# Kernel optimization log

Hardware: AMD Instinct MI355X
Metric: run time of the kernel (lower is better)

## Reference

```python
import jax, jax.numpy as jnp
import numpy as np

B, S, H, D = 8, 4096, 1024, 256  # batch, seq, hidden_size, state_size


def setup_inputs() -> dict:
    key = jax.random.key(0)
    ks = jax.random.split(key, 4)
    scale_in = 1.0 / np.sqrt(H)
    scale_st = 1.0 / np.sqrt(D)
    return {
        "x": jax.random.normal(ks[0], (B, S, H), dtype=jnp.float32),
        "W_in": jax.random.normal(ks[1], (H, D), dtype=jnp.float32) * scale_in,
        "b_in": jnp.zeros((D,), dtype=jnp.float32),
        "W_state": jax.random.normal(ks[2], (D, D), dtype=jnp.float32) * scale_st,
        "b_state": jnp.zeros((D,), dtype=jnp.float32),
        "W_out": jax.random.normal(ks[3], (D, H), dtype=jnp.float32) * scale_st,
        "b_out": jnp.zeros((H,), dtype=jnp.float32),
    }


def reference(x, W_in, b_in, W_state, b_state, W_out, b_out):
    # Precompute input projection for all timesteps in one big GEMM: [B,S,D]
    inp = jnp.einsum("bsh,hd->bsd", x, W_in) + b_in

    def step(state, inp_t):
        # state: [B,D], inp_t: [B,D]
        state = jnp.tanh(inp_t + state @ W_state + b_state)
        return state, state

    state0 = jnp.zeros((x.shape[0], W_state.shape[0]), dtype=x.dtype)
    # scan over time axis -> states: [S,B,D]
    _, states = jax.lax.scan(step, state0, jnp.swapaxes(inp, 0, 1))
    # output projection: [S,B,H] -> [B,S,H]
    out = jnp.einsum("sbd,dh->sbh", states, W_out) + b_out
    return jnp.swapaxes(out, 0, 1)
```

## Files before the change

kernel.cpp:

```cpp
#include <hip/hip_runtime.h>
#include <stdint.h>


typedef float v4f __attribute__((ext_vector_type(4)));
typedef __bf16 bf16x4 __attribute__((ext_vector_type(4)));
typedef __bf16 bf16x8 __attribute__((ext_vector_type(8)));
typedef _Float16 h8 __attribute__((ext_vector_type(8)));

#define BARRIER_LGKM() asm volatile("s_waitcnt lgkmcnt(0)\n\ts_barrier" ::: "memory")

#define GLOAD_LDS16(g, l)                                                    \
  __builtin_amdgcn_global_load_lds(                                          \
      (const __attribute__((address_space(1))) void*)(g),                    \
      (__attribute__((address_space(3))) void*)(l), 16, 0, 0)

__global__ void cvt_f32_bf16_x4(const float* __restrict__ in,
                                __bf16* __restrict__ out, int n4) {
  int i = blockIdx.x * blockDim.x + threadIdx.x;
  if (i >= n4) return;
  v4f v = ((const v4f*)in)[i];
  bf16x4 o;
  o.x = (__bf16)v.x; o.y = (__bf16)v.y; o.z = (__bf16)v.z; o.w = (__bf16)v.w;
  ((bf16x4*)out)[i] = o;
}

__global__ void transpose_cvt(const float* __restrict__ in,
                              __bf16* __restrict__ out, int K, int N) {
  int i = blockIdx.x * blockDim.x + threadIdx.x;
  if (i >= K * N) return;
  int k = i / N;
  int n = i - k * N;
  out[(size_t)n * K + k] = (__bf16)in[i];
}

__global__ __launch_bounds__(256) void gemm_tile(
    const __bf16* __restrict__ A,
    const __bf16* __restrict__ Bt,
    const float* __restrict__ bias,
    float* __restrict__ C,
    int M, int N, int K) {
  const int tid = threadIdx.x;
  const int lane = tid & 63;
  const int w = tid >> 6;
  const int wr = w >> 1, wc = w & 1;
  const int r = lane & 15, q = lane >> 4;

  const int nbn = N >> 7;
  const int mb = blockIdx.x / nbn;
  const int nb = blockIdx.x - mb * nbn;
  const int m0 = mb << 7, n0 = nb << 7;

  __shared__ __align__(16) char lds[2][16384];

  const __bf16* gA[2];
  const __bf16* gB[2];
  int loff[2];
#pragma unroll
  for (int j = 0; j < 2; ++j) {
    int o = (w * 2 + j) * 1024 + lane * 16;
    int row = o >> 6;
    int s = (o >> 4) & 3;
    int ss = s ^ ((row >> 1) & 3);
    gA[j] = A + (size_t)(m0 + row) * K + ss * 8;
    gB[j] = Bt + (size_t)(n0 + row) * K + ss * 8;
    loff[j] = (w * 2 + j) * 1024;
  }

  const int slot = (q ^ ((r >> 1) & 3)) * 16;
  int aoff[4], boff[4];
#pragma unroll
  for (int i = 0; i < 4; ++i) {
    aoff[i] = (wr * 64 + i * 16 + r) * 64 + slot;
    boff[i] = 8192 + (wc * 64 + i * 16 + r) * 64 + slot;
  }

  v4f acc[4][4];
#pragma unroll
  for (int mi = 0; mi < 4; ++mi)
#pragma unroll
    for (int ni = 0; ni < 4; ++ni) acc[mi][ni] = (v4f){0.f, 0.f, 0.f, 0.f};

  const int NK = K >> 5;
#pragma unroll
  for (int j = 0; j < 2; ++j) {
    GLOAD_LDS16(gA[j], lds[0] + loff[j]);
    GLOAD_LDS16(gB[j], lds[0] + 8192 + loff[j]);
  }

  for (int kt = 0; kt < NK; ++kt) {
    __syncthreads();
    if (kt + 1 < NK) {
      const int b = (kt + 1) & 1;
      const int ke = (kt + 1) * 32;
#pragma unroll
      for (int j = 0; j < 2; ++j) {
        GLOAD_LDS16(gA[j] + ke, lds[b] + loff[j]);
        GLOAD_LDS16(gB[j] + ke, lds[b] + 8192 + loff[j]);
      }
    }
    const char* Lb = lds[kt & 1];
    bf16x8 af[4], bf[4];
#pragma unroll
    for (int i = 0; i < 4; ++i) af[i] = *(const bf16x8*)(Lb + aoff[i]);
#pragma unroll
    for (int i = 0; i < 4; ++i) bf[i] = *(const bf16x8*)(Lb + boff[i]);
#pragma unroll
    for (int mi = 0; mi < 4; ++mi)
#pragma unroll
      for (int ni = 0; ni < 4; ++ni)
        acc[mi][ni] = __builtin_amdgcn_mfma_f32_16x16x32_bf16(
            af[mi], bf[ni], acc[mi][ni], 0, 0, 0);
  }

  float bv[4];
#pragma unroll
  for (int ni = 0; ni < 4; ++ni) bv[ni] = bias[n0 + wc * 64 + ni * 16 + r];
#pragma unroll
  for (int mi = 0; mi < 4; ++mi) {
    int rowb = m0 + wr * 64 + mi * 16 + q * 4;
#pragma unroll
    for (int ni = 0; ni < 4; ++ni) {
      int col = n0 + wc * 64 + ni * 16 + r;
      float* cp = C + (size_t)rowb * N + col;
#pragma unroll
      for (int i = 0; i < 4; ++i) cp[(size_t)i * N] = acc[mi][ni][i] + bv[ni];
    }
  }
}

__global__ __launch_bounds__(512, 2) void scan_mfma(
    const float* __restrict__ inp,
    const float* __restrict__ Wst,
    const float* __restrict__ b_state,
    __bf16* __restrict__ states,
    int S) {
  const int tid = threadIdx.x;
  const int l = tid & 63;
  const int q = l >> 4;
  const int r = l & 15;
  const int w = tid >> 6;
  const int b = blockIdx.x;

  __shared__ __align__(16) _Float16 sbuf[2][256];

  h8 bwA[8], bwB[8];
#pragma unroll
  for (int c = 0; c < 8; ++c) {
#pragma unroll
    for (int i = 0; i < 8; ++i) {
      const float* wp = Wst + (size_t)(32 * c + 8 * q + i) * 256 + 32 * w + r;
      bwA[c][i] = (_Float16)wp[0];
      bwB[c][i] = (_Float16)wp[16];
    }
  }

  const int col = 32 * w + 16 * (q & 1) + r;
  const float bst = b_state[col];
  const float* inpb = inp + (size_t)b * S * 256;
  __bf16* stb = states + (size_t)b * S * 256;

  if (tid < 256) sbuf[0][tid] = (_Float16)0.f;
  float u_cur = inpb[col];
  float u_nxt = inpb[256 + col];
  __syncthreads();

  int cur = 0;
  for (int t = 0; t < S; ++t) {
    float u_n2 = 0.f;
    if (t + 2 < S) u_n2 = inpb[(size_t)(t + 2) * 256 + col];

    const h8* sp = (const h8*)sbuf[cur];
    h8 af[8];
#pragma unroll
    for (int c = 0; c < 8; ++c) af[c] = sp[4 * c + q];

    v4f a0 = {0.f, 0.f, 0.f, 0.f};
    v4f a1 = a0;
#pragma unroll
    for (int c = 0; c < 8; ++c) {
      a0 = __builtin_amdgcn_mfma_f32_16x16x32_f16(af[c], bwA[c], a0, 0, 0, 0);
      a1 = __builtin_amdgcn_mfma_f32_16x16x32_f16(af[c], bwB[c], a1, 0, 0, 0);
    }
    float x = ((q & 1) ? a1[0] : a0[0]) + u_cur + bst;

    float e = exp2f(2.885390082f * x);
    float sn = 1.f - 2.f * __builtin_amdgcn_rcpf(e + 1.f);

    cur ^= 1;
    if (q < 2) {
      sbuf[cur][col] = (_Float16)sn;
      stb[(size_t)t * 256 + col] = (__bf16)sn;
    }
    u_cur = u_nxt;
    u_nxt = u_n2;
    BARRIER_LGKM();
  }
}

extern "C" void kernel_launch(void* const* d_in, const int* in_sizes, int n_in,
                              void* d_out, int out_size, void* d_ws,
                              size_t ws_size, hipStream_t stream) {
  const float* x       = (const float*)d_in[0];
  const float* W_in    = (const float*)d_in[1];
  const float* b_in    = (const float*)d_in[2];
  const float* W_state = (const float*)d_in[3];
  const float* b_state = (const float*)d_in[4];
  const float* W_out   = (const float*)d_in[5];
  const float* b_out   = (const float*)d_in[6];
  float* out = (float*)d_out;

  const int B = 8, S = 4096, H = 1024, D = 256;
  const int M = B * S;

  char* ws = (char*)d_ws;
  float*  inp    = (float*)(ws + 0);
  __bf16* states = (__bf16*)(ws + 33554432);
  __bf16* xb     = (__bf16*)(ws + 50331648);
  __bf16* WinT   = (__bf16*)(ws + 117440512);
  __bf16* WoutT  = (__bf16*)(ws + 117964800);

  cvt_f32_bf16_x4<<<(M * H / 4 + 255) / 256, 256, 0, stream>>>(x, xb, M * H / 4);
  transpose_cvt<<<(H * D + 255) / 256, 256, 0, stream>>>(W_in, WinT, H, D);
  transpose_cvt<<<(D * H + 255) / 256, 256, 0, stream>>>(W_out, WoutT, D, H);

  gemm_tile<<<(M / 128) * (D / 128), 256, 0, stream>>>(xb, WinT, b_in, inp, M, D, H);

  scan_mfma<<<B, 512, 0, stream>>>(inp, W_state, b_state, states, S);

  gemm_tile<<<(M / 128) * (H / 128), 256, 0, stream>>>(states, WoutT, b_out, out, M, H, D);
}
```

Baseline: 2.113 ms.

## Split scan recurrence across 16 waves with one 16-column tile each

The sequential scan kernel now runs 1024 threads (16 waves) per batch element instead of 8. Each wave owns a single 16-column output tile, and the eight MFMAs are split across two independent accumulators, shortening the dependent MFMA chain per timestep. The intent is to cut per-step latency on the serial recurrence. The cost is a barrier across more waves every step and fewer lanes doing writes. The GEMM variable rename is cosmetic.

After: 2.106 ms. Within noise of the previous version (-0.3%).

```diff
diff --git a/kernel.cpp b/kernel.cpp
--- a/kernel.cpp
+++ b/kernel.cpp
@@ -90,12 +90,12 @@
   for (int kt = 0; kt < NK; ++kt) {
     __syncthreads();
     if (kt + 1 < NK) {
-      const int b = (kt + 1) & 1;
+      const int bb = (kt + 1) & 1;
       const int ke = (kt + 1) * 32;
 #pragma unroll
       for (int j = 0; j < 2; ++j) {
-        GLOAD_LDS16(gA[j] + ke, lds[b] + loff[j]);
-        GLOAD_LDS16(gB[j] + ke, lds[b] + 8192 + loff[j]);
+        GLOAD_LDS16(gA[j] + ke, lds[bb] + loff[j]);
+        GLOAD_LDS16(gB[j] + ke, lds[bb] + 8192 + loff[j]);
       }
     }
     const char* Lb = lds[kt & 1];
@@ -128,7 +128,7 @@
   }
 }
 
-__global__ __launch_bounds__(512, 2) void scan_mfma(
+__global__ __launch_bounds__(1024) void scan_mfma(
     const float* __restrict__ inp,
     const float* __restrict__ Wst,
     const float* __restrict__ b_state,
@@ -143,18 +143,15 @@
 
   __shared__ __align__(16) _Float16 sbuf[2][256];
 
-  h8 bwA[8], bwB[8];
+  h8 bw[8];
 #pragma unroll
   for (int c = 0; c < 8; ++c) {
 #pragma unroll
-    for (int i = 0; i < 8; ++i) {
-      const float* wp = Wst + (size_t)(32 * c + 8 * q + i) * 256 + 32 * w + r;
-      bwA[c][i] = (_Float16)wp[0];
-      bwB[c][i] = (_Float16)wp[16];
-    }
-  }
-
-  const int col = 32 * w + 16 * (q & 1) + r;
+    for (int i = 0; i < 8; ++i)
+      bw[c][i] = (_Float16)Wst[(size_t)(32 * c + 8 * q + i) * 256 + 16 * w + r];
+  }
+
+  const int col = 16 * w + r;
   const float bst = b_state[col];
   const float* inpb = inp + (size_t)b * S * 256;
   __bf16* stb = states + (size_t)b * S * 256;
@@ -174,20 +171,20 @@
 #pragma unroll
     for (int c = 0; c < 8; ++c) af[c] = sp[4 * c + q];
 
-    v4f a0 = {0.f, 0.f, 0.f, 0.f};
-    v4f a1 = a0;
-#pragma unroll
-    for (int c = 0; c < 8; ++c) {
-      a0 = __builtin_amdgcn_mfma_f32_16x16x32_f16(af[c], bwA[c], a0, 0, 0, 0);
-      a1 = __builtin_amdgcn_mfma_f32_16x16x32_f16(af[c], bwB[c], a1, 0, 0, 0);
-    }
-    float x = ((q & 1) ? a1[0] : a0[0]) + u_cur + bst;
+    v4f accE = {0.f, 0.f, 0.f, 0.f};
+    v4f accO = accE;
+#pragma unroll
+    for (int c = 0; c < 4; ++c) {
+      accE = __builtin_amdgcn_mfma_f32_16x16x32_f16(af[2 * c],     bw[2 * c],     accE, 0, 0, 0);
+      accO = __builtin_amdgcn_mfma_f32_16x16x32_f16(af[2 * c + 1], bw[2 * c + 1], accO, 0, 0, 0);
+    }
+    float x = accE[0] + accO[0] + u_cur + bst;
 
     float e = exp2f(2.885390082f * x);
     float sn = 1.f - 2.f * __builtin_amdgcn_rcpf(e + 1.f);
 
     cur ^= 1;
-    if (q < 2) {
+    if (q == 0) {
       sbuf[cur][col] = (_Float16)sn;
       stb[(size_t)t * 256 + col] = (__bf16)sn;
     }
@@ -225,7 +222,7 @@
 
   gemm_tile<<<(M / 128) * (D / 128), 256, 0, stream>>>(xb, WinT, b_in, inp, M, D, H);
 
-  scan_mfma<<<B, 512, 0, stream>>>(inp, W_state, b_state, states, S);
+  scan_mfma<<<B, 1024, 0, stream>>>(inp, W_state, b_state, states, S);
 
   gemm_tile<<<(M / 128) * (H / 128), 256, 0, stream>>>(states, WoutT, b_out, out, M, H, D);
 }
```

## Fuse input GEMM, scan and output GEMM into one persistent kernel with flags

Applied to the files above, without the earlier changes.

Replaces the three separate launches (input-projection GEMM, sequential scan, output-projection GEMM) with one persistent kernel. Eight blocks run the scan while the other blocks pull work items from an atomic counter, producing input-projection chunks ahead of the scan and consuming finished state chunks for the output GEMM. Progress and readiness are passed through global flags with acquire/release fences. This hides the two GEMMs behind the latency-bound scan. Worker blocks sharing a CU with a scan block are told to exit so they do not slow it, at the cost of spin-wait and fence overhead in the scan loop every 128 steps.

Measured after the change: 2.293 ms. 1.09x slower.

```diff
diff --git a/kernel.cpp b/kernel.cpp
--- a/kernel.cpp
+++ b/kernel.cpp
@@ -13,6 +13,22 @@
   __builtin_amdgcn_global_load_lds(                                          \
       (const __attribute__((address_space(1))) void*)(g),                    \
       (__attribute__((address_space(3))) void*)(l), 16, 0, 0)
+
+#define GETREG_HWID  __builtin_amdgcn_s_getreg(0xF804)
+#define GETREG_XCCID __builtin_amdgcn_s_getreg(0xF814)
+
+#define AT_LOAD(p)     __hip_atomic_load((p), __ATOMIC_RELAXED, __HIP_MEMORY_SCOPE_AGENT)
+#define AT_STORE(p, v) __hip_atomic_store((p), (v), __ATOMIC_RELAXED, __HIP_MEMORY_SCOPE_AGENT)
+#define AT_ADD(p, v)   __hip_atomic_fetch_add((p), (v), __ATOMIC_RELAXED, __HIP_MEMORY_SCOPE_AGENT)
+#define FENCE_ACQ() __builtin_amdgcn_fence(__ATOMIC_ACQUIRE, "agent")
+#define FENCE_REL() __builtin_amdgcn_fence(__ATOMIC_RELEASE, "agent")
+
+#define CTL_NEXT 0
+#define CTL_REG  1
+#define CTL_PROG 2
+#define CTL_SCU  10
+#define CTL_EXIT 18
+#define CTL_G1   32
 
 __global__ void cvt_f32_bf16_x4(const float* __restrict__ in,
                                 __bf16* __restrict__ out, int n4) {
@@ -33,24 +49,16 @@
   out[(size_t)n * K + k] = (__bf16)in[i];
 }
 
-__global__ __launch_bounds__(256) void gemm_tile(
-    const __bf16* __restrict__ A,
-    const __bf16* __restrict__ Bt,
-    const float* __restrict__ bias,
-    float* __restrict__ C,
-    int M, int N, int K) {
-  const int tid = threadIdx.x;
+__global__ void zero_ctl(uint32_t* p) { p[threadIdx.x] = 0; }
+
+__device__ __forceinline__ void gemm128(
+    const __bf16* __restrict__ A, const __bf16* __restrict__ Bt,
+    const float* __restrict__ bias, float* __restrict__ C,
+    int N, int K, int m0, int n0, char* lds, int tid) {
   const int lane = tid & 63;
   const int w = tid >> 6;
   const int wr = w >> 1, wc = w & 1;
   const int r = lane & 15, q = lane >> 4;
-
-  const int nbn = N >> 7;
-  const int mb = blockIdx.x / nbn;
-  const int nb = blockIdx.x - mb * nbn;
-  const int m0 = mb << 7, n0 = nb << 7;
-
-  __shared__ __align__(16) char lds[2][16384];
 
   const __bf16* gA[2];
   const __bf16* gB[2];
@@ -83,22 +91,22 @@
   const int NK = K >> 5;
 #pragma unroll
   for (int j = 0; j < 2; ++j) {
-    GLOAD_LDS16(gA[j], lds[0] + loff[j]);
-    GLOAD_LDS16(gB[j], lds[0] + 8192 + loff[j]);
+    GLOAD_LDS16(gA[j], lds + loff[j]);
+    GLOAD_LDS16(gB[j], lds + 8192 + loff[j]);
   }
 
   for (int kt = 0; kt < NK; ++kt) {
     __syncthreads();
     if (kt + 1 < NK) {
-      const int b = (kt + 1) & 1;
+      char* lb = lds + ((kt + 1) & 1) * 16384;
       const int ke = (kt + 1) * 32;
 #pragma unroll
       for (int j = 0; j < 2; ++j) {
-        GLOAD_LDS16(gA[j] + ke, lds[b] + loff[j]);
-        GLOAD_LDS16(gB[j] + ke, lds[b] + 8192 + loff[j]);
-      }
-    }
-    const char* Lb = lds[kt & 1];
+        GLOAD_LDS16(gA[j] + ke, lb + loff[j]);
+        GLOAD_LDS16(gB[j] + ke, lb + 8192 + loff[j]);
+      }
+    }
+    const char* Lb = lds + (kt & 1) * 16384;
     bf16x8 af[4], bf[4];
 #pragma unroll
     for (int i = 0; i < 4; ++i) af[i] = *(const bf16x8*)(Lb + aoff[i]);
@@ -128,72 +136,167 @@
   }
 }
 
-__global__ __launch_bounds__(512, 2) void scan_mfma(
-    const float* __restrict__ inp,
+__global__ __launch_bounds__(512) void fused(
+    const __bf16* __restrict__ xb,
+    const __bf16* __restrict__ WinT,
+    const float* __restrict__ b_in,
+    float* __restrict__ inp,
     const float* __restrict__ Wst,
     const float* __restrict__ b_state,
     __bf16* __restrict__ states,
-    int S) {
+    const __bf16* __restrict__ WoutT,
+    const float* __restrict__ b_out,
+    float* __restrict__ out,
+    uint32_t* __restrict__ ctl, int S) {
   const int tid = threadIdx.x;
-  const int l = tid & 63;
-  const int q = l >> 4;
-  const int r = l & 15;
-  const int w = tid >> 6;
-  const int b = blockIdx.x;
-
-  __shared__ __align__(16) _Float16 sbuf[2][256];
-
-  h8 bwA[8], bwB[8];
-#pragma unroll
-  for (int c = 0; c < 8; ++c) {
-#pragma unroll
-    for (int i = 0; i < 8; ++i) {
-      const float* wp = Wst + (size_t)(32 * c + 8 * q + i) * 256 + 32 * w + r;
-      bwA[c][i] = (_Float16)wp[0];
-      bwB[c][i] = (_Float16)wp[16];
-    }
-  }
-
-  const int col = 32 * w + 16 * (q & 1) + r;
-  const float bst = b_state[col];
-  const float* inpb = inp + (size_t)b * S * 256;
-  __bf16* stb = states + (size_t)b * S * 256;
-
-  if (tid < 256) sbuf[0][tid] = (_Float16)0.f;
-  float u_cur = inpb[col];
-  float u_nxt = inpb[256 + col];
-  __syncthreads();
-
-  int cur = 0;
-  for (int t = 0; t < S; ++t) {
-    float u_n2 = 0.f;
-    if (t + 2 < S) u_n2 = inpb[(size_t)(t + 2) * 256 + col];
-
-    const h8* sp = (const h8*)sbuf[cur];
-    h8 af[8];
-#pragma unroll
-    for (int c = 0; c < 8; ++c) af[c] = sp[4 * c + q];
-
-    v4f a0 = {0.f, 0.f, 0.f, 0.f};
-    v4f a1 = a0;
+  __shared__ __align__(16) char ldsAll[65552];
+
+  uint32_t* progress = ctl + CTL_PROG;
+  uint32_t* scanCU = ctl + CTL_SCU;
+  uint32_t* g1flag = ctl + CTL_G1;
+
+  if (blockIdx.x < 8) {
+    const int b = blockIdx.x;
+    const int l = tid & 63;
+    const int q = l >> 4;
+    const int r = l & 15;
+    const int w = tid >> 6;
+
+    if (tid == 0) {
+      uint32_t id = ((GETREG_HWID >> 8) & 0xFF) | (GETREG_XCCID << 8);
+      AT_STORE(&scanCU[b], id);
+      __hip_atomic_fetch_add(&ctl[CTL_REG], 1u, __ATOMIC_RELEASE,
+                             __HIP_MEMORY_SCOPE_AGENT);
+    }
+
+    h8 bwA[8], bwB[8];
 #pragma unroll
     for (int c = 0; c < 8; ++c) {
-      a0 = __builtin_amdgcn_mfma_f32_16x16x32_f16(af[c], bwA[c], a0, 0, 0, 0);
-      a1 = __builtin_amdgcn_mfma_f32_16x16x32_f16(af[c], bwB[c], a1, 0, 0, 0);
-    }
-    float x = ((q & 1) ? a1[0] : a0[0]) + u_cur + bst;
-
-    float e = exp2f(2.885390082f * x);
-    float sn = 1.f - 2.f * __builtin_amdgcn_rcpf(e + 1.f);
-
-    cur ^= 1;
-    if (q < 2) {
-      sbuf[cur][col] = (_Float16)sn;
-      stb[(size_t)t * 256 + col] = (__bf16)sn;
-    }
-    u_cur = u_nxt;
-    u_nxt = u_n2;
-    BARRIER_LGKM();
+#pragma unroll
+      for (int i = 0; i < 8; ++i) {
+        const float* wp = Wst + (size_t)(32 * c + 8 * q + i) * 256 + 32 * w + r;
+        bwA[c][i] = (_Float16)wp[0];
+        bwB[c][i] = (_Float16)wp[16];
+      }
+    }
+
+    const int col = 32 * w + 16 * (q & 1) + r;
+    const float bst = b_state[col];
+    const float* inpb = inp + (size_t)b * S * 256;
+    __bf16* stb = states + (size_t)b * S * 256;
+
+    if (tid == 0) {
+      while (AT_LOAD(&g1flag[b]) == 0) __builtin_amdgcn_s_sleep(8);
+    }
+    __syncthreads();
+    FENCE_ACQ();
+
+    _Float16* sbuf = (_Float16*)ldsAll;
+    if (tid < 256) sbuf[tid] = (_Float16)0.f;
+    float u_cur = inpb[col];
+    float u_nxt = inpb[256 + col];
+    __syncthreads();
+
+    int cur = 0;
+    for (int t = 0; t < S; ++t) {
+      if ((t + 2 < S) && (((t + 2) & 127) == 0)) {
+        const int c = (t + 2) >> 7;
+        if (tid == 0) {
+          while (AT_LOAD(&g1flag[c * 8 + b]) == 0) __builtin_amdgcn_s_sleep(8);
+        }
+        __syncthreads();
+        FENCE_ACQ();
+      }
+      float u_n2 = 0.f;
+      if (t + 2 < S) u_n2 = inpb[(size_t)(t + 2) * 256 + col];
+
+      const h8* sp = (const h8*)(ldsAll + cur * 512);
+      h8 af[8];
+#pragma unroll
+      for (int c = 0; c < 8; ++c) af[c] = sp[4 * c + q];
+
+      v4f a0 = {0.f, 0.f, 0.f, 0.f};
+      v4f a1 = a0;
+#pragma unroll
+      for (int c = 0; c < 8; ++c) {
+        a0 = __builtin_amdgcn_mfma_f32_16x16x32_f16(af[c], bwA[c], a0, 0, 0, 0);
+        a1 = __builtin_amdgcn_mfma_f32_16x16x32_f16(af[c], bwB[c], a1, 0, 0, 0);
+      }
+      float x = ((q & 1) ? a1[0] : a0[0]) + u_cur + bst;
+
+      float e = exp2f(2.885390082f * x);
+      float sn = 1.f - 2.f * __builtin_amdgcn_rcpf(e + 1.f);
+
+      cur ^= 1;
+      if (q < 2) {
+        ((_Float16*)ldsAll)[cur * 256 + col] = (_Float16)sn;
+        stb[(size_t)t * 256 + col] = (__bf16)sn;
+      }
+      if ((t & 127) == 127) {
+        asm volatile("s_waitcnt vmcnt(0)" ::: "memory");
+        __syncthreads();
+        if (tid == 0) {
+          FENCE_REL();
+          AT_STORE(&progress[b], (uint32_t)(t + 1));
+        }
+      }
+      u_cur = u_nxt;
+      u_nxt = u_n2;
+      BARRIER_LGKM();
+    }
+  } else {
+    volatile uint32_t* bc = (volatile uint32_t*)(ldsAll + 65536);
+    if (tid == 0) {
+      while (__hip_atomic_load(&ctl[CTL_REG], __ATOMIC_ACQUIRE,
+                               __HIP_MEMORY_SCOPE_AGENT) < 8)
+        __builtin_amdgcn_s_sleep(8);
+      uint32_t id = ((GETREG_HWID >> 8) & 0xFF) | (GETREG_XCCID << 8);
+      uint32_t clash = 0;
+#pragma unroll
+      for (int i = 0; i < 8; ++i)
+        if (AT_LOAD(&scanCU[i]) == id) clash = 1;
+      uint32_t doexit = 0;
+      if (clash && AT_ADD(&ctl[CTL_EXIT], 1u) < 16) doexit = 1;
+      *bc = doexit;
+    }
+    __syncthreads();
+    if (*bc) return;
+
+    const int sub = tid >> 8;
+    const int stid = tid & 255;
+    char* myl = ldsAll + sub * 32768;
+
+    for (;;) {
+      __syncthreads();
+      if (tid == 0) *bc = AT_ADD(&ctl[CTL_NEXT], 1u);
+      __syncthreads();
+      uint32_t P = *bc;
+      if (P >= 1280) return;
+
+      if (P < 256) {
+        const int c = P >> 3, b = P & 7;
+        const int m0 = b * 4096 + c * 128;
+        gemm128(xb, WinT, b_in, inp, 256, 1024, m0, sub * 128, myl, stid);
+        asm volatile("s_waitcnt vmcnt(0)" ::: "memory");
+        __syncthreads();
+        if (tid == 0) {
+          FENCE_REL();
+          AT_STORE(&g1flag[P], 1u);
+        }
+      } else {
+        const uint32_t Q = P - 256;
+        const int mc = Q >> 5, b = (Q >> 2) & 7, np = Q & 3;
+        if (tid == 0) {
+          const uint32_t need = (uint32_t)(mc + 1) * 128;
+          while (AT_LOAD(&progress[b]) < need) __builtin_amdgcn_s_sleep(64);
+        }
+        __syncthreads();
+        FENCE_ACQ();
+        const int m0 = b * 4096 + mc * 128;
+        gemm128(states, WoutT, b_out, out, 1024, 256, m0,
+                (np * 2 + sub) * 128, myl, stid);
+      }
+    }
   }
 }
 
@@ -218,14 +321,13 @@
   __bf16* xb     = (__bf16*)(ws + 50331648);
   __bf16* WinT   = (__bf16*)(ws + 117440512);
   __bf16* WoutT  = (__bf16*)(ws + 117964800);
+  uint32_t* ctl  = (uint32_t*)(ws + 118489088);
 
   cvt_f32_bf16_x4<<<(M * H / 4 + 255) / 256, 256, 0, stream>>>(x, xb, M * H / 4);
   transpose_cvt<<<(H * D + 255) / 256, 256, 0, stream>>>(W_in, WinT, H, D);
   transpose_cvt<<<(D * H + 255) / 256, 256, 0, stream>>>(W_out, WoutT, D, H);
-
-  gemm_tile<<<(M / 128) * (D / 128), 256, 0, stream>>>(xb, WinT, b_in, inp, M, D, H);
-
-  scan_mfma<<<B, 512, 0, stream>>>(inp, W_state, b_state, states, S);
-
-  gemm_tile<<<(M / 128) * (H / 128), 256, 0, stream>>>(states, WoutT, b_out, out, M, H, D);
-}
+  zero_ctl<<<1, 512, 0, stream>>>(ctl);
+
+  fused<<<248, 512, 0, stream>>>(xb, WinT, b_in, inp, W_state, b_state,
+                                 states, WoutT, b_out, out, ctl, S);
+}
```
